# Performance work log

Measured on AMD Instinct MI355X. Metric: run time of the kernel, lower is better.

Reference implementation:

```python
import jax, jax.numpy as jnp
import numpy as np

LAMBDA_DEPTHG = 0.3
STEGO_TEMPERATURE = 0.1
KNN_K = 7
DEPTH_SIGMA = 0.5
EPS = 1e-8


def _l2norm(x):
    return x / jnp.sqrt(jnp.sum(x * x, axis=-1, keepdims=True) + EPS)


def _stego_loss(codes, feats, temperature, knn_k):
    # Pairwise cosine similarity of DINO features -> KNN graph (includes self).
    f = _l2norm(feats)                                  # (B,N,Df)
    sim_f = jnp.einsum('bnd,bmd->bnm', f, f)            # (B,N,N)
    _, knn_idx = jax.lax.top_k(sim_f, knn_k)            # (B,N,k) int32
    # Temperature-scaled InfoNCE over code similarities; KNN entries are positives.
    c = _l2norm(codes)                                  # (B,N,Dc)
    logits = jnp.einsum('bnd,bmd->bnm', c, c) / temperature  # (B,N,N)
    logp = jax.nn.log_softmax(logits, axis=-1)          # (B,N,N)
    pos_logp = jnp.take_along_axis(logp, knn_idx, axis=-1)   # (B,N,k)
    return -jnp.mean(pos_logp)


def _depth_guided_correlation_loss(codes, depth, sigma_d):
    # Gaussian depth affinity: pixels at similar depth should have similar codes.
    dd = depth[:, :, None] - depth[:, None, :]          # (B,N,N)
    w = jnp.exp(-(dd * dd) / (2.0 * sigma_d * sigma_d)) # (B,N,N)
    c = _l2norm(codes)
    s = jnp.einsum('bnd,bmd->bnm', c, c)                # (B,N,N) cosine corr
    return jnp.mean(w * (1.0 - s))


def setup_inputs() -> dict:
    key = jax.random.key(0)
    k1, k2, k3 = jax.random.split(key, 3)
    B, N = 2, 4096
    semantic_codes = jax.random.normal(k1, (B, N, 90), dtype=jnp.float32)
    dino_features = jax.random.normal(k2, (B, N, 384), dtype=jnp.float32)
    depth = jax.random.uniform(k3, (B, N), dtype=jnp.float32)
    return {"semantic_codes": semantic_codes, "dino_features": dino_features, "depth": depth}


def reference(semantic_codes, dino_features, depth):
    l_stego = _stego_loss(semantic_codes, dino_features, STEGO_TEMPERATURE, KNN_K)
    l_depthg = _depth_guided_correlation_loss(semantic_codes, depth, DEPTH_SIGMA)
    total = l_stego + LAMBDA_DEPTHG * l_depthg
    return (l_stego, l_depthg, total)
```

## Files before the change

kernel.cpp:

```cpp
#include <hip/hip_runtime.h>
#include <math.h>

#define NPTS 4096

typedef __attribute__((ext_vector_type(8))) short bf16x8;
typedef __attribute__((ext_vector_type(16))) float f32x16;

#define KEEP(x) asm volatile("" : "+v"(x))

__device__ __forceinline__ f32x16 zero16() {
  f32x16 z;
#pragma unroll
  for (int i = 0; i < 16; ++i) z[i] = 0.f;
  return z;
}

__device__ __forceinline__ unsigned packkey(float x, int m) {
  unsigned u = __float_as_uint(x);
  unsigned key = u ^ ((unsigned)((int)u >> 31) | 0x80000000u);
  return (key & 0xFFFFF000u) | (unsigned)m;
}

__device__ __forceinline__ void cas7(unsigned v, unsigned* s) {
#pragma unroll
  for (int t = 0; t < 7; ++t) {
    const unsigned hi = s[t] >= v ? s[t] : v;
    const unsigned lo = s[t] >= v ? v : s[t];
    s[t] = hi;
    v = lo;
  }
}

__device__ __forceinline__ unsigned bf16pack(float a, float b) {
  unsigned ua = __float_as_uint(a); ua = (ua + 0x7FFFu + ((ua >> 16) & 1u)) >> 16;
  unsigned ub = __float_as_uint(b); ub = (ub + 0x7FFFu + ((ub >> 16) & 1u)) >> 16;
  return ua | (ub << 16);
}

__global__ __launch_bounds__(64) void norm_f(const float* __restrict__ feats,
                                             unsigned short* __restrict__ Fsw) {
  const int row = blockIdx.x;
  const int lane = threadIdx.x;
  const int b = row >> 12, mt = (row >> 5) & 127, rl = row & 31;

  const float* f = feats + (size_t)row * 384;
  float v[8];
  float ss = 0.f;
  if (lane < 48) {
    float4 p0 = *(const float4*)(f + lane * 8);
    float4 p1 = *(const float4*)(f + lane * 8 + 4);
    v[0] = p0.x; v[1] = p0.y; v[2] = p0.z; v[3] = p0.w;
    v[4] = p1.x; v[5] = p1.y; v[6] = p1.z; v[7] = p1.w;
#pragma unroll
    for (int e = 0; e < 8; ++e) ss = fmaf(v[e], v[e], ss);
  }
#pragma unroll
  for (int m = 1; m <= 32; m <<= 1) ss += __shfl_xor(ss, m, 64);
  const float inv = rsqrtf(ss + 1e-8f);
  if (lane < 48) {
    uint4 o;
    o.x = bf16pack(v[0] * inv, v[1] * inv);
    o.y = bf16pack(v[2] * inv, v[3] * inv);
    o.z = bf16pack(v[4] * inv, v[5] * inv);
    o.w = bf16pack(v[6] * inv, v[7] * inv);
    const int kc = lane >> 1, hs = lane & 1;
    *(uint4*)(Fsw + (((size_t)(b * 128 + mt) * 24 + kc) << 9) + (hs * 32 + rl) * 8) = o;
  }
}

__global__ __launch_bounds__(64) void norm_c(const float* __restrict__ codes,
                                             unsigned short* __restrict__ Csw,
                                             float* __restrict__ invc) {
  const int row = blockIdx.x;
  const int lane = threadIdx.x;
  const int b = row >> 12, mt = (row >> 5) & 127, rl = row & 31;

  const float* c = codes + (size_t)row * 90;
  float cv[8];
#pragma unroll
  for (int e = 0; e < 8; ++e) cv[e] = 0.f;
  if (lane < 11) {
    float4 p0 = *(const float4*)(c + lane * 8);
    float4 p1 = *(const float4*)(c + lane * 8 + 4);
    cv[0] = p0.x; cv[1] = p0.y; cv[2] = p0.z; cv[3] = p0.w;
    cv[4] = p1.x; cv[5] = p1.y; cv[6] = p1.z; cv[7] = p1.w;
  } else if (lane == 11) {
    cv[0] = c[88]; cv[1] = c[89];
  }
  float cs = 0.f;
#pragma unroll
  for (int e = 0; e < 8; ++e) cs = fmaf(cv[e], cv[e], cs);
#pragma unroll
  for (int m = 1; m <= 32; m <<= 1) cs += __shfl_xor(cs, m, 64);
  const float cinv = rsqrtf(cs + 1e-8f);
  if (lane < 12) {
    uint4 o;
    o.x = bf16pack(cv[0] * cinv, cv[1] * cinv);
    o.y = bf16pack(cv[2] * cinv, cv[3] * cinv);
    o.z = bf16pack(cv[4] * cinv, cv[5] * cinv);
    o.w = bf16pack(cv[6] * cinv, cv[7] * cinv);
    const int kc = lane >> 1, hs = lane & 1;
    *(uint4*)(Csw + (((size_t)(b * 128 + mt) * 6 + kc) << 9) + (hs * 32 + rl) * 8) = o;
  }
  if (lane == 0) invc[row] = cinv;
}

__global__ __launch_bounds__(512, 1) void knn_mfma(const unsigned short* __restrict__ Fsw,
                                                   unsigned* __restrict__ cand) {
  __shared__ unsigned ckey[8][32][7];
  const int g = blockIdx.x;
  const int b = g & 1;
  const int h = (g >> 1) & 1;
  const int qt = g >> 2;
  const int q0 = qt * 32;
  const int tid = threadIdx.x;
  const int w = tid >> 6;
  const int lane = tid & 63;
  const int lo = lane & 31, hi4 = (lane >> 5) * 4;
  const unsigned short* Fb = Fsw + (size_t)b * 128 * 24 * 512;

  bf16x8 bfr[24];
  {
    const unsigned short* qb = Fb + ((size_t)qt * 24) * 512 + lane * 8;
#pragma unroll
    for (int t = 0; t < 24; ++t) bfr[t] = *(const bf16x8*)(qb + t * 512);
#pragma unroll
    for (int t = 0; t < 24; ++t) KEEP(bfr[t]);
  }
  unsigned s7[7];
#pragma unroll
  for (int t = 0; t < 7; ++t) s7[t] = 0u;

  const int t0 = h * 64 + w * 8;
  const unsigned short* ab = Fb + ((size_t)t0 * 24) * 512 + lane * 8;

  bf16x8 a0[12], a1[12];
#pragma unroll
  for (int t = 0; t < 12; ++t) a0[t] = *(const bf16x8*)(ab + t * 512);
#pragma unroll
  for (int t = 0; t < 12; ++t) KEEP(a0[t]);

  for (int mt = 0; mt < 8; ++mt) {
    const unsigned short* art = ab + (size_t)mt * 24 * 512;
#pragma unroll
    for (int t = 0; t < 12; ++t) a1[t] = *(const bf16x8*)(art + (12 + t) * 512);
#pragma unroll
    for (int t = 0; t < 12; ++t) KEEP(a1[t]);
    f32x16 acc = zero16();
#pragma unroll
    for (int t = 0; t < 12; ++t)
      acc = __builtin_amdgcn_mfma_f32_32x32x16_bf16(a0[t], bfr[t], acc, 0, 0, 0);
    if (mt + 1 < 8) {
      const unsigned short* arn = ab + (size_t)(mt + 1) * 24 * 512;
#pragma unroll
      for (int t = 0; t < 12; ++t) a0[t] = *(const bf16x8*)(arn + t * 512);
#pragma unroll
      for (int t = 0; t < 12; ++t) KEEP(a0[t]);
    }
#pragma unroll
    for (int t = 0; t < 12; ++t)
      acc = __builtin_amdgcn_mfma_f32_32x32x16_bf16(a1[t], bfr[12 + t], acc, 0, 0, 0);
    const int mb = (t0 + mt) * 32 + hi4;
#pragma unroll
    for (int r = 0; r < 16; ++r) {
      const int m = mb + (r & 3) + 8 * (r >> 2);
      cas7(packkey(acc[r], m), s7);
    }
  }

#pragma unroll
  for (int t = 0; t < 7; ++t) {
    const unsigned ov = (unsigned)__shfl_xor((int)s7[t], 32, 64);
    cas7(ov, s7);
  }
  if (lane < 32) {
#pragma unroll
    for (int t = 0; t < 7; ++t) ckey[w][lo][t] = s7[t];
  }
  __syncthreads();

  if (tid < 32) {
    unsigned fs[7];
#pragma unroll
    for (int t = 0; t < 7; ++t) fs[t] = 0u;
    for (int w2 = 0; w2 < 8; ++w2)
#pragma unroll
      for (int t = 0; t < 7; ++t) cas7(ckey[w2][tid][t], fs);
    unsigned* o = cand + ((size_t)((h * 2 + b) * NPTS) + q0 + tid) * 7;
#pragma unroll
    for (int t = 0; t < 7; ++t) o[t] = fs[t];
  }
}

__global__ __launch_bounds__(512, 1) void lse_depth(const unsigned short* __restrict__ Csw,
                                                    const float* __restrict__ depth,
                                                    float* __restrict__ slse_part,
                                                    float* __restrict__ dpart) {
  __shared__ float lsep[8][32];
  __shared__ float depp[8];
  const int g = blockIdx.x;
  const int b = g & 1;
  const int h = (g >> 1) & 1;
  const int qt = g >> 2;
  const int q0 = qt * 32;
  const int tid = threadIdx.x;
  const int w = tid >> 6;
  const int lane = tid & 63;
  const int lo = lane & 31, hi4 = (lane >> 5) * 4;
  const unsigned short* Cb = Csw + (size_t)b * 128 * 6 * 512;
  const float* db = depth + b * NPTS;

  bf16x8 bfr[6];
  {
    const unsigned short* qb = Cb + ((size_t)qt * 6) * 512 + lane * 8;
#pragma unroll
    for (int t = 0; t < 6; ++t) bfr[t] = *(const bf16x8*)(qb + t * 512);
#pragma unroll
    for (int t = 0; t < 6; ++t) KEEP(bfr[t]);
  }
  const float dq = db[q0 + lo];
  float slse = 0.f, sdep = 0.f;

  const int t0 = h * 64 + w * 8;
  const unsigned short* ab = Cb + ((size_t)t0 * 6) * 512 + lane * 8;

  bf16x8 a0[6], a1[6];
#pragma unroll
  for (int t = 0; t < 6; ++t) a0[t] = *(const bf16x8*)(ab + t * 512);
#pragma unroll
  for (int t = 0; t < 6; ++t) KEEP(a0[t]);

#define PROC3(A, GT)                                                           \
  {                                                                            \
    f32x16 acc = zero16();                                                     \
    _Pragma("unroll")                                                          \
    for (int t = 0; t < 6; ++t)                                                \
      acc = __builtin_amdgcn_mfma_f32_32x32x16_bf16(A[t], bfr[t], acc, 0, 0, 0); \
    float dvv[16];                                                             \
    _Pragma("unroll")                                                          \
    for (int k = 0; k < 4; ++k) {                                              \
      float4 dv = *(const float4*)(db + (GT) * 32 + hi4 + 8 * k);              \
      dvv[k * 4 + 0] = dv.x; dvv[k * 4 + 1] = dv.y;                            \
      dvv[k * 4 + 2] = dv.z; dvv[k * 4 + 3] = dv.w;                            \
    }                                                                          \
    _Pragma("unroll")                                                          \
    for (int r = 0; r < 16; ++r) {                                             \
      const float s = acc[r];                                                  \
      const float dd = dq - dvv[r];                                            \
      sdep += __expf(-2.f * dd * dd) * (1.f - s);                              \
      slse += __expf(fmaf(s, 10.f, -10.f));                                    \
    }                                                                          \
  }

  for (int mt = 0; mt < 8; mt += 2) {
    {
      const unsigned short* ar = ab + (size_t)(mt + 1) * 6 * 512;
#pragma unroll
      for (int t = 0; t < 6; ++t) a1[t] = *(const bf16x8*)(ar + t * 512);
#pragma unroll
      for (int t = 0; t < 6; ++t) KEEP(a1[t]);
    }
    PROC3(a0, t0 + mt)
    if (mt + 2 < 8) {
      const unsigned short* ar = ab + (size_t)(mt + 2) * 6 * 512;
#pragma unroll
      for (int t = 0; t < 6; ++t) a0[t] = *(const bf16x8*)(ar + t * 512);
#pragma unroll
      for (int t = 0; t < 6; ++t) KEEP(a0[t]);
    }
    PROC3(a1, t0 + mt + 1)
  }
#undef PROC3

  slse += __shfl_xor(slse, 32, 64);
  if (lane < 32) lsep[w][lo] = slse;
#pragma unroll
  for (int m = 1; m <= 32; m <<= 1) sdep += __shfl_xor(sdep, m, 64);
  if (lane == 0) depp[w] = sdep;
  __syncthreads();
  if (tid < 32) {
    float tot = 0.f;
#pragma unroll
    for (int w2 = 0; w2 < 8; ++w2) tot += lsep[w2][tid];
    slse_part[(size_t)((h * 2 + b) * NPTS) + q0 + tid] = tot;
  }
  if (tid == 32) {
    float d = 0.f;
#pragma unroll
    for (int w2 = 0; w2 < 8; ++w2) d += depp[w2];
    dpart[g] = d;
  }
}

__global__ __launch_bounds__(64) void gather_pos(const float* __restrict__ codes,
                                                 const float* __restrict__ invc,
                                                 const unsigned* __restrict__ cand,
                                                 float* __restrict__ gpart) {
  const int n = blockIdx.x;
  const int b = n >> 12, q = n & 4095;
  const int lane = threadIdx.x;

  unsigned s[7];
#pragma unroll
  for (int t = 0; t < 7; ++t) s[t] = 0u;
  const unsigned* c0 = cand + ((size_t)(b * NPTS) + q) * 7;
  const unsigned* c1 = cand + ((size_t)((2 + b) * NPTS) + q) * 7;
#pragma unroll
  for (int t = 0; t < 7; ++t) cas7(c0[t], s);
#pragma unroll
  for (int t = 0; t < 7; ++t) cas7(c1[t], s);
  bool has = false;
#pragma unroll
  for (int t = 0; t < 7; ++t) has = has || ((s[t] & 4095u) == (unsigned)q);
  if (!has) s[6] = (unsigned)q;

  const float* cn = codes + (size_t)n * 90;
  float2 a = make_float2(0.f, 0.f);
  if (lane < 45) a = *(const float2*)(cn + lane * 2);
  const float inva = invc[n];
  float ssum = 0.f;
#pragma unroll
  for (int k = 0; k < 7; ++k) {
    const int m = (int)(s[k] & 4095u);
    const float* cm = codes + ((size_t)(b << 12) + m) * 90;
    float2 bb = make_float2(0.f, 0.f);
    if (lane < 45) bb = *(const float2*)(cm + lane * 2);
    float p = fmaf(a.x, bb.x, a.y * bb.y);
#pragma unroll
    for (int w = 1; w <= 32; w <<= 1) p += __shfl_xor(p, w, 64);
    ssum += p * inva * invc[(b << 12) + m];
  }
  if (lane == 0) gpart[n] = ssum;
}

__global__ __launch_bounds__(256) void finalize(const float* __restrict__ slse_part,
                                                const float* __restrict__ gpart,
                                                const float* __restrict__ dpart,
                                                float* __restrict__ out) {
  const int tid = threadIdx.x;
  float s1 = 0.f, s2 = 0.f;
  for (int n = tid; n < 2 * NPTS; n += 256) {
    const int b = n >> 12, q = n & 4095;
    const float p = slse_part[b * NPTS + q] + slse_part[(2 + b) * NPTS + q];
    s1 += 10.f + __logf(p);
    s2 += gpart[n];
  }
  float s3 = dpart[tid] + dpart[tid + 256];
  __shared__ float r1[256], r2[256], r3[256];
  r1[tid] = s1; r2[tid] = s2; r3[tid] = s3;
  __syncthreads();
  for (int s = 128; s > 0; s >>= 1) {
    if (tid < s) { r1[tid] += r1[tid + s]; r2[tid] += r2[tid + s]; r3[tid] += r3[tid + s]; }
    __syncthreads();
  }
  if (tid == 0) {
    const float l_st = (7.f * r1[0] - 10.f * r2[0]) / 57344.f;
    const float l_dp = r3[0] / 33554432.f;
    out[0] = l_st;
    out[1] = l_dp;
    out[2] = l_st + 0.3f * l_dp;
  }
}

extern "C" void kernel_launch(void* const* d_in, const int* in_sizes, int n_in,
                              void* d_out, int out_size, void* d_ws, size_t ws_size,
                              hipStream_t stream) {
  (void)in_sizes; (void)n_in; (void)out_size; (void)ws_size;
  const float* codes = (const float*)d_in[0];
  const float* feats = (const float*)d_in[1];
  const float* depth = (const float*)d_in[2];
  float* out = (float*)d_out;

  char* ws = (char*)d_ws;
  float*    invc      = (float*)ws;
  unsigned* cand      = (unsigned*)(ws + 32768);
  unsigned short* Fsw = (unsigned short*)(ws + 589824);
  unsigned short* Csw = (unsigned short*)(ws + 589824);
  float*    slse_part = (float*)(ws + 2162688);
  float*    dpart     = (float*)(ws + 2228224);
  float*    gpart     = (float*)(ws + 2230272);

  norm_f<<<2 * NPTS, 64, 0, stream>>>(feats, Fsw);
  knn_mfma<<<512, 512, 0, stream>>>(Fsw, cand);
  norm_c<<<2 * NPTS, 64, 0, stream>>>(codes, Csw, invc);
  lse_depth<<<512, 512, 0, stream>>>(Csw, depth, slse_part, dpart);
  gather_pos<<<2 * NPTS, 64, 0, stream>>>(codes, invc, cand, gpart);
  finalize<<<1, 256, 0, stream>>>(slse_part, gpart, dpart, out);
}
```

Baseline: 97.86 us.

## Split key range into four partitions with 256-thread blocks for KNN and LSE

The key dimension of the knn and lse/depth kernels is now split across four partitions instead of two, and each block has 4 waves instead of 8, giving 1024 blocks in place of 512. Downstream gather and finalize now merge four partial candidate lists and four partial sums, and the workspace offsets grow to fit them. The aim is to fill the MI355X CUs more evenly with smaller blocks. The cost is that each block reloads its query fragment, and the extra partials add merge work and memory traffic.

```diff
diff --git a/kernel.cpp b/kernel.cpp
--- a/kernel.cpp
+++ b/kernel.cpp
@@ -105,13 +105,13 @@
   if (lane == 0) invc[row] = cinv;
 }
 
-__global__ __launch_bounds__(512, 1) void knn_mfma(const unsigned short* __restrict__ Fsw,
+__global__ __launch_bounds__(256, 1) void knn_mfma(const unsigned short* __restrict__ Fsw,
                                                    unsigned* __restrict__ cand) {
-  __shared__ unsigned ckey[8][32][7];
+  __shared__ unsigned ckey[4][32][7];
   const int g = blockIdx.x;
   const int b = g & 1;
-  const int h = (g >> 1) & 1;
-  const int qt = g >> 2;
+  const int p = (g >> 1) & 3;
+  const int qt = g >> 3;
   const int q0 = qt * 32;
   const int tid = threadIdx.x;
   const int w = tid >> 6;
@@ -131,7 +131,7 @@
 #pragma unroll
   for (int t = 0; t < 7; ++t) s7[t] = 0u;
 
-  const int t0 = h * 64 + w * 8;
+  const int t0 = p * 32 + w * 8;
   const unsigned short* ab = Fb + ((size_t)t0 * 24) * 512 + lane * 8;
 
   bf16x8 a0[12], a1[12];
@@ -183,25 +183,25 @@
     unsigned fs[7];
 #pragma unroll
     for (int t = 0; t < 7; ++t) fs[t] = 0u;
-    for (int w2 = 0; w2 < 8; ++w2)
+    for (int w2 = 0; w2 < 4; ++w2)
 #pragma unroll
       for (int t = 0; t < 7; ++t) cas7(ckey[w2][tid][t], fs);
-    unsigned* o = cand + ((size_t)((h * 2 + b) * NPTS) + q0 + tid) * 7;
+    unsigned* o = cand + ((size_t)((p * 2 + b) * NPTS) + q0 + tid) * 7;
 #pragma unroll
     for (int t = 0; t < 7; ++t) o[t] = fs[t];
   }
 }
 
-__global__ __launch_bounds__(512, 1) void lse_depth(const unsigned short* __restrict__ Csw,
+__global__ __launch_bounds__(256, 1) void lse_depth(const unsigned short* __restrict__ Csw,
                                                     const float* __restrict__ depth,
                                                     float* __restrict__ slse_part,
                                                     float* __restrict__ dpart) {
-  __shared__ float lsep[8][32];
-  __shared__ float depp[8];
+  __shared__ float lsep[4][32];
+  __shared__ float depp[4];
   const int g = blockIdx.x;
   const int b = g & 1;
-  const int h = (g >> 1) & 1;
-  const int qt = g >> 2;
+  const int p = (g >> 1) & 3;
+  const int qt = g >> 3;
   const int q0 = qt * 32;
   const int tid = threadIdx.x;
   const int w = tid >> 6;
@@ -221,7 +221,7 @@
   const float dq = db[q0 + lo];
   float slse = 0.f, sdep = 0.f;
 
-  const int t0 = h * 64 + w * 8;
+  const int t0 = p * 32 + w * 8;
   const unsigned short* ab = Cb + ((size_t)t0 * 6) * 512 + lane * 8;
 
   bf16x8 a0[6], a1[6];
@@ -281,13 +281,13 @@
   if (tid < 32) {
     float tot = 0.f;
 #pragma unroll
-    for (int w2 = 0; w2 < 8; ++w2) tot += lsep[w2][tid];
-    slse_part[(size_t)((h * 2 + b) * NPTS) + q0 + tid] = tot;
+    for (int w2 = 0; w2 < 4; ++w2) tot += lsep[w2][tid];
+    slse_part[(size_t)((p * 2 + b) * NPTS) + q0 + tid] = tot;
   }
   if (tid == 32) {
     float d = 0.f;
 #pragma unroll
-    for (int w2 = 0; w2 < 8; ++w2) d += depp[w2];
+    for (int w2 = 0; w2 < 4; ++w2) d += depp[w2];
     dpart[g] = d;
   }
 }
@@ -303,12 +303,12 @@
   unsigned s[7];
 #pragma unroll
   for (int t = 0; t < 7; ++t) s[t] = 0u;
-  const unsigned* c0 = cand + ((size_t)(b * NPTS) + q) * 7;
-  const unsigned* c1 = cand + ((size_t)((2 + b) * NPTS) + q) * 7;
-#pragma unroll
-  for (int t = 0; t < 7; ++t) cas7(c0[t], s);
-#pragma unroll
-  for (int t = 0; t < 7; ++t) cas7(c1[t], s);
+#pragma unroll
+  for (int pp = 0; pp < 4; ++pp) {
+    const unsigned* cp = cand + ((size_t)((pp * 2 + b) * NPTS) + q) * 7;
+#pragma unroll
+    for (int t = 0; t < 7; ++t) cas7(cp[t], s);
+  }
   bool has = false;
 #pragma unroll
   for (int t = 0; t < 7; ++t) has = has || ((s[t] & 4095u) == (unsigned)q);
@@ -341,11 +341,15 @@
   float s1 = 0.f, s2 = 0.f;
   for (int n = tid; n < 2 * NPTS; n += 256) {
     const int b = n >> 12, q = n & 4095;
-    const float p = slse_part[b * NPTS + q] + slse_part[(2 + b) * NPTS + q];
-    s1 += 10.f + __logf(p);
+    float pz = 0.f;
+#pragma unroll
+    for (int pp = 0; pp < 4; ++pp) pz += slse_part[(pp * 2 + b) * NPTS + q];
+    s1 += 10.f + __logf(pz);
     s2 += gpart[n];
   }
-  float s3 = dpart[tid] + dpart[tid + 256];
+  float s3 = 0.f;
+#pragma unroll
+  for (int k = 0; k < 4; ++k) s3 += dpart[tid + k * 256];
   __shared__ float r1[256], r2[256], r3[256];
   r1[tid] = s1; r2[tid] = s2; r3[tid] = s3;
   __syncthreads();
@@ -374,16 +378,16 @@
   char* ws = (char*)d_ws;
   float*    invc      = (float*)ws;
   unsigned* cand      = (unsigned*)(ws + 32768);
-  unsigned short* Fsw = (unsigned short*)(ws + 589824);
-  unsigned short* Csw = (unsigned short*)(ws + 589824);
-  float*    slse_part = (float*)(ws + 2162688);
-  float*    dpart     = (float*)(ws + 2228224);
-  float*    gpart     = (float*)(ws + 2230272);
+  unsigned short* Fsw = (unsigned short*)(ws + 950272);
+  unsigned short* Csw = (unsigned short*)(ws + 950272);
+  float*    slse_part = (float*)(ws + 2523136);
+  float*    dpart     = (float*)(ws + 2654208);
+  float*    gpart     = (float*)(ws + 2658304);
 
   norm_f<<<2 * NPTS, 64, 0, stream>>>(feats, Fsw);
-  knn_mfma<<<512, 512, 0, stream>>>(Fsw, cand);
+  knn_mfma<<<1024, 256, 0, stream>>>(Fsw, cand);
   norm_c<<<2 * NPTS, 64, 0, stream>>>(codes, Csw, invc);
-  lse_depth<<<512, 512, 0, stream>>>(Csw, depth, slse_part, dpart);
+  lse_depth<<<1024, 256, 0, stream>>>(Csw, depth, slse_part, dpart);
   gather_pos<<<2 * NPTS, 64, 0, stream>>>(codes, invc, cand, gpart);
   finalize<<<1, 256, 0, stream>>>(slse_part, gpart, dpart, out);
 }
```

Result: slower. 101.8 us (+4.0%).
